# Kernel optimization log

Measured on AMD Instinct MI355X. Metric: run time of the kernel, lower is better.

Reference implementation:

```python
import jax, jax.numpy as jnp
import numpy as np

POOL_SIZE = 7
CROP = POOL_SIZE * 2  # if_max_pool=True -> crop to 14x14 then 2x2 max-pool


def setup_inputs() -> dict:
    key = jax.random.key(0)
    k1, k2, k3 = jax.random.split(key, 3)
    H, W, C = 50, 75, 512          # VGG conv5 features of an 800x1200 image (stride 16)
    N = 1000                       # post-NMS RPN proposals
    feature_map = jax.random.normal(k1, (1, H, W, C), dtype=jnp.float32)
    img_size = jnp.array([800, 1200], dtype=jnp.int32)
    # rois in pixel coords (x1, y1, x2, y2), guaranteed x1<=x2, y1<=y2, in-bounds
    xs = jax.random.uniform(k2, (N, 2), minval=0.0, maxval=1199.0)
    ys = jax.random.uniform(k3, (N, 2), minval=0.0, maxval=799.0)
    rois = jnp.stack([xs.min(1), ys.min(1), xs.max(1), ys.max(1)], axis=1).astype(jnp.float32)
    return {"feature_map": feature_map, "rois": rois, "img_size": img_size}


def _crop_and_resize(feature_map, boxes, crop_h, crop_w):
    """tf.image.crop_and_resize (bilinear) with all box_indices == 0.
    feature_map: (1,H,W,C); boxes: (N,4) normalized [y1,x1,y2,x2].
    Returns (N, crop_h, crop_w, C).
    """
    H, W = feature_map.shape[1], feature_map.shape[2]
    img = feature_map[0]  # (H,W,C)
    y1, x1, y2, x2 = boxes[:, 0], boxes[:, 1], boxes[:, 2], boxes[:, 3]
    fh, fw = jnp.float32(H - 1), jnp.float32(W - 1)
    iy = jnp.arange(crop_h, dtype=jnp.float32)
    ix = jnp.arange(crop_w, dtype=jnp.float32)
    # in-image sample coords (crop size > 1 branch of TF semantics)
    ys = y1[:, None] * fh + iy[None, :] * ((y2 - y1) * fh / (crop_h - 1))[:, None]  # (N,ch)
    xs = x1[:, None] * fw + ix[None, :] * ((x2 - x1) * fw / (crop_w - 1))[:, None]  # (N,cw)
    valid = ((ys >= 0) & (ys <= fh))[:, :, None] & ((xs >= 0) & (xs <= fw))[:, None, :]  # (N,ch,cw)
    y0 = jnp.floor(ys); x0 = jnp.floor(xs)
    wy = (ys - y0)[:, :, None, None]   # (N,ch,1,1)
    wx = (xs - x0)[:, None, :, None]   # (N,1,cw,1)
    y0i = jnp.clip(y0.astype(jnp.int32), 0, H - 1)
    x0i = jnp.clip(x0.astype(jnp.int32), 0, W - 1)
    y1i = jnp.clip(y0i + 1, 0, H - 1)
    x1i = jnp.clip(x0i + 1, 0, W - 1)
    # per-ROI bilinear gather: (N,ch,cw,C)
    tl = img[y0i[:, :, None], x0i[:, None, :]]
    tr = img[y0i[:, :, None], x1i[:, None, :]]
    bl = img[y1i[:, :, None], x0i[:, None, :]]
    br = img[y1i[:, :, None], x1i[:, None, :]]
    top = tl + wx * (tr - tl)
    bot = bl + wx * (br - bl)
    val = top + wy * (bot - top)
    return jnp.where(valid[..., None], val, 0.0)


def reference(feature_map, rois, img_size):
    img_h = img_size[0].astype(jnp.float32) - 1.0
    img_w = img_size[1].astype(jnp.float32) - 1.0
    boxes = jnp.stack([rois[:, 1] / img_h, rois[:, 0] / img_w,
                       rois[:, 3] / img_h, rois[:, 2] / img_w], axis=1)
    boxes = jax.lax.stop_gradient(boxes)
    crops = _crop_and_resize(feature_map, boxes, CROP, CROP)  # (N,14,14,C)
    N, _, _, C = crops.shape
    # MaxPool2D((2,2), padding='same'); 14 is even so 'same' == 'valid' reshape trick
    return crops.reshape(N, POOL_SIZE, 2, POOL_SIZE, 2, C).max(axis=(2, 4))
```

## Files before the change

### kernel.cpp

```cpp
#include <hip/hip_runtime.h>

#define FH 50
#define FW 75
#define FC 512
#define NPOOL 7
#define NXCD 8
#define NSAMP 14

typedef float f32x4 __attribute__((ext_vector_type(4)));
typedef int   i32x4 __attribute__((ext_vector_type(4)));

__global__ __launch_bounds__(256) void roi_setup_kernel(
    const float* __restrict__ rois,
    const int*   __restrict__ img_size,
    i32x4* __restrict__ tab,
    int N)
{
    const int idx = blockIdx.x * 256 + threadIdx.x;
    const int total = N * NSAMP;
    if (idx >= 2 * total) return;

    const bool is_col = idx >= total;
    const int  e = is_col ? idx - total : idx;
    const int  n = e / NSAMP;
    const int  j = e % NSAMP;

    if (!is_col) {
        const float img_h = (float)(img_size[0] - 1);
        const float ry1 = rois[n * 4 + 1];
        const float ry2 = rois[n * 4 + 3];
        const float fh = (float)(FH - 1);
        const float stepy = (ry2 - ry1) / img_h * fh * (1.0f / 13.0f);
        const float basey = ry1 / img_h * fh;
        const float ys = basey + (float)j * stepy;
        const float my = ((ys >= 0.0f) & (ys <= fh)) ? 1.0f : 0.0f;
        const float y0f = floorf(ys);
        const float wy = ys - y0f;
        int y0 = min(max((int)y0f, 0), FH - 1);
        int y1 = min(y0 + 1, FH - 1);
        i32x4 v;
        v.x = y0 * (FW * FC);
        v.y = y1 * (FW * FC);
        v.z = __float_as_int((1.0f - wy) * my);
        v.w = __float_as_int(wy * my);
        tab[e] = v;
    } else {
        const float img_w = (float)(img_size[1] - 1);
        const float rx1 = rois[n * 4 + 0];
        const float rx2 = rois[n * 4 + 2];
        const float fw = (float)(FW - 1);
        const float stepx = (rx2 - rx1) / img_w * fw * (1.0f / 13.0f);
        const float basex = rx1 / img_w * fw;
        const float xs = basex + (float)j * stepx;
        const float mx = ((xs >= 0.0f) & (xs <= fw)) ? 1.0f : 0.0f;
        const float x0f = floorf(xs);
        const float wx = xs - x0f;
        int x0 = min(max((int)x0f, 0), FW - 1);
        int x1 = min(x0 + 1, FW - 1);
        i32x4 v;
        v.x = x0 * FC;
        v.y = x1 * FC;
        v.z = __float_as_int((1.0f - wx) * mx);
        v.w = __float_as_int(wx * mx);
        tab[total + e] = v;
    }
}

__global__ __launch_bounds__(128) void roi_pool_kernel(
    const float* __restrict__ fmap,
    const i32x4* __restrict__ tab,
    float* __restrict__ out,
    int N)
{
    const int nwg = gridDim.x;
    const int q = nwg / NXCD, r = nwg % NXCD;
    const int xcd = blockIdx.x % NXCD, local = blockIdx.x / NXCD;
    const int w = (xcd < r ? xcd * (q + 1) : r * (q + 1) + (xcd - r) * q) + local;

    const int n  = w / (NPOOL * NPOOL);
    const int p  = w % (NPOOL * NPOOL);
    const int py = p / NPOOL;
    const int px = p % NPOOL;
    if (n >= N) return;

    const int ri = __builtin_amdgcn_readfirstlane(n * NSAMP + 2 * py);
    const int ci = __builtin_amdgcn_readfirstlane(N * NSAMP + n * NSAMP + 2 * px);
    const i32x4 R0 = tab[ri];
    const i32x4 R1 = tab[ri + 1];
    const i32x4 C0 = tab[ci];
    const i32x4 C1 = tab[ci + 1];

    const float r0a = __int_as_float(R0.z), r0b = __int_as_float(R0.w);
    const float r1a = __int_as_float(R1.z), r1b = __int_as_float(R1.w);
    const float c0a = __int_as_float(C0.z), c0b = __int_as_float(C0.w);
    const float c1a = __int_as_float(C1.z), c1b = __int_as_float(C1.w);

    const int c4 = threadIdx.x * 4;
    const float* fm = fmap + c4;

    const f32x4 s00a = *(const f32x4*)(fm + R0.x + C0.x);
    const f32x4 s00b = *(const f32x4*)(fm + R0.x + C0.y);
    const f32x4 s00c = *(const f32x4*)(fm + R0.y + C0.x);
    const f32x4 s00d = *(const f32x4*)(fm + R0.y + C0.y);
    const f32x4 s01a = *(const f32x4*)(fm + R0.x + C1.x);
    const f32x4 s01b = *(const f32x4*)(fm + R0.x + C1.y);
    const f32x4 s01c = *(const f32x4*)(fm + R0.y + C1.x);
    const f32x4 s01d = *(const f32x4*)(fm + R0.y + C1.y);
    const f32x4 s10a = *(const f32x4*)(fm + R1.x + C0.x);
    const f32x4 s10b = *(const f32x4*)(fm + R1.x + C0.y);
    const f32x4 s10c = *(const f32x4*)(fm + R1.y + C0.x);
    const f32x4 s10d = *(const f32x4*)(fm + R1.y + C0.y);
    const f32x4 s11a = *(const f32x4*)(fm + R1.x + C1.x);
    const f32x4 s11b = *(const f32x4*)(fm + R1.x + C1.y);
    const f32x4 s11c = *(const f32x4*)(fm + R1.y + C1.x);
    const f32x4 s11d = *(const f32x4*)(fm + R1.y + C1.y);

    const f32x4 v00 = (r0a*c0a)*s00a + (r0a*c0b)*s00b + (r0b*c0a)*s00c + (r0b*c0b)*s00d;
    const f32x4 v01 = (r0a*c1a)*s01a + (r0a*c1b)*s01b + (r0b*c1a)*s01c + (r0b*c1b)*s01d;
    const f32x4 v10 = (r1a*c0a)*s10a + (r1a*c0b)*s10b + (r1b*c0a)*s10c + (r1b*c0b)*s10d;
    const f32x4 v11 = (r1a*c1a)*s11a + (r1a*c1b)*s11b + (r1b*c1a)*s11c + (r1b*c1b)*s11d;

    f32x4 m;
    m.x = fmaxf(fmaxf(fmaxf(v00.x, v01.x), v10.x), v11.x);
    m.y = fmaxf(fmaxf(fmaxf(v00.y, v01.y), v10.y), v11.y);
    m.z = fmaxf(fmaxf(fmaxf(v00.z, v01.z), v10.z), v11.z);
    m.w = fmaxf(fmaxf(fmaxf(v00.w, v01.w), v10.w), v11.w);

    f32x4* dst = (f32x4*)(out + (((long)n * NPOOL + py) * NPOOL + px) * FC + c4);
    __builtin_nontemporal_store(m, dst);
}

extern "C" void kernel_launch(void* const* d_in, const int* in_sizes, int n_in,
                              void* d_out, int out_size, void* d_ws, size_t ws_size,
                              hipStream_t stream) {
    const float* fmap     = (const float*)d_in[0];
    const float* rois     = (const float*)d_in[1];
    const int*   img_size = (const int*)d_in[2];
    float* out = (float*)d_out;

    const int N = in_sizes[1] / 4;
    i32x4* tab = (i32x4*)d_ws;

    const int setup_threads = 2 * N * NSAMP;
    roi_setup_kernel<<<(setup_threads + 255) / 256, 256, 0, stream>>>(
        rois, img_size, tab, N);

    const int blocks = N * NPOOL * NPOOL;
    roi_pool_kernel<<<blocks, 128, 0, stream>>>(fmap, tab, out, N);
}
```

Before: 162.6 us.

## Sort ROIs by vertical center so each XCD gathers nearby feature rows

Adds a single-block bitonic sort kernel that orders ROIs by y1+y2. The pool kernel then maps workgroups through this permutation, so each XCD's contiguous chunk handles ROIs with similar vertical positions. The goal is better L2 locality for the gathered feature-map rows. The cost is an extra serial kernel launch with about 55 barrier steps, plus one extra indirection load per workgroup.

```diff
diff --git a/kernel.cpp b/kernel.cpp
--- a/kernel.cpp
+++ b/kernel.cpp
@@ -6,6 +6,8 @@
 #define NPOOL 7
 #define NXCD 8
 #define NSAMP 14
+#define SORT_SIZE 1024
+#define SORT_THREADS 512
 
 typedef float f32x4 __attribute__((ext_vector_type(4)));
 typedef int   i32x4 __attribute__((ext_vector_type(4)));
@@ -66,9 +68,51 @@
     }
 }
 
+__global__ __launch_bounds__(SORT_THREADS) void roi_sort_kernel(
+    const float* __restrict__ rois, int* __restrict__ perm, int N)
+{
+    __shared__ float key[SORT_SIZE];
+    __shared__ int   idx[SORT_SIZE];
+    const int t = threadIdx.x;
+
+    if (N > SORT_SIZE) {
+        for (int i = t; i < N; i += SORT_THREADS) perm[i] = i;
+        return;
+    }
+
+    #pragma unroll
+    for (int s = 0; s < 2; ++s) {
+        const int e = t + s * SORT_THREADS;
+        key[e] = (e < N) ? (rois[e * 4 + 1] + rois[e * 4 + 3]) : INFINITY;
+        idx[e] = e;
+    }
+    __syncthreads();
+
+    for (int size = 2; size <= SORT_SIZE; size <<= 1) {
+        for (int stride = size >> 1; stride > 0; stride >>= 1) {
+            const int lo  = ((t & ~(stride - 1)) << 1) | (t & (stride - 1));
+            const int hi  = lo | stride;
+            const bool up = ((lo & size) == 0);
+            const float ka = key[lo], kb = key[hi];
+            const int   ia = idx[lo], ib = idx[hi];
+            if (up ? (ka > kb) : (ka < kb)) {
+                key[lo] = kb; key[hi] = ka;
+                idx[lo] = ib; idx[hi] = ia;
+            }
+            __syncthreads();
+        }
+    }
+    #pragma unroll
+    for (int s = 0; s < 2; ++s) {
+        const int e = t + s * SORT_THREADS;
+        if (e < N) perm[e] = idx[e];
+    }
+}
+
 __global__ __launch_bounds__(128) void roi_pool_kernel(
     const float* __restrict__ fmap,
     const i32x4* __restrict__ tab,
+    const int*   __restrict__ perm,
     float* __restrict__ out,
     int N)
 {
@@ -77,11 +121,13 @@
     const int xcd = blockIdx.x % NXCD, local = blockIdx.x / NXCD;
     const int w = (xcd < r ? xcd * (q + 1) : r * (q + 1) + (xcd - r) * q) + local;
 
-    const int n  = w / (NPOOL * NPOOL);
+    const int ns = w / (NPOOL * NPOOL);
     const int p  = w % (NPOOL * NPOOL);
     const int py = p / NPOOL;
     const int px = p % NPOOL;
-    if (n >= N) return;
+    if (ns >= N) return;
+
+    const int n = perm[__builtin_amdgcn_readfirstlane(ns)];
 
     const int ri = __builtin_amdgcn_readfirstlane(n * NSAMP + 2 * py);
     const int ci = __builtin_amdgcn_readfirstlane(N * NSAMP + n * NSAMP + 2 * px);
@@ -139,12 +185,14 @@
     float* out = (float*)d_out;
 
     const int N = in_sizes[1] / 4;
-    i32x4* tab = (i32x4*)d_ws;
+    i32x4* tab  = (i32x4*)d_ws;
+    int*   perm = (int*)(tab + 2 * N * NSAMP);
 
     const int setup_threads = 2 * N * NSAMP;
     roi_setup_kernel<<<(setup_threads + 255) / 256, 256, 0, stream>>>(
         rois, img_size, tab, N);
+    roi_sort_kernel<<<1, SORT_THREADS, 0, stream>>>(rois, perm, N);
 
     const int blocks = N * NPOOL * NPOOL;
-    roi_pool_kernel<<<blocks, 128, 0, stream>>>(fmap, tab, out, N);
+    roi_pool_kernel<<<blocks, 128, 0, stream>>>(fmap, tab, perm, out, N);
 }
```

Result: slower. 174.1 us (+7.1%).
